# Kernel optimization log

Hardware: AMD Instinct MI355X
Metric: run time of the kernel (lower is better)

Reference implementation:

```python
import jax, jax.numpy as jnp
import numpy as np

D_MODEL = 1024


def setup_inputs() -> dict:
    key = jax.random.key(0)
    ks = jax.random.split(key, 7)
    s = 1.0 / np.sqrt(D_MODEL)
    return {
        "x": jax.random.normal(ks[0], (4, 4096, D_MODEL), dtype=jnp.float32),
        "Wq": jax.random.normal(ks[1], (D_MODEL, D_MODEL), dtype=jnp.float32) * s,
        "bq": jax.random.normal(ks[2], (D_MODEL,), dtype=jnp.float32) * s,
        "Wk": jax.random.normal(ks[3], (D_MODEL, D_MODEL), dtype=jnp.float32) * s,
        "bk": jax.random.normal(ks[4], (D_MODEL,), dtype=jnp.float32) * s,
        "Wv": jax.random.normal(ks[5], (D_MODEL, D_MODEL), dtype=jnp.float32) * s,
        "bv": jax.random.normal(ks[6], (D_MODEL,), dtype=jnp.float32) * s,
    }


def reference(x, Wq, bq, Wk, bk, Wv, bv):
    # nn.Linear: y = x @ W.T + b
    Q = jnp.einsum("bsd,ed->bse", x, Wq) + bq  # [B,S,D]
    K = jnp.einsum("bsd,ed->bse", x, Wk) + bk
    V = jnp.einsum("bsd,ed->bse", x, Wv) + bv
    scale = 1.0 / jnp.sqrt(jnp.asarray(x.shape[-1], dtype=x.dtype))
    KV = jnp.einsum("bsd,bse->bde", K, V) * scale  # [B,D,D]
    E = jnp.einsum("bsd,bde->bse", Q, KV)  # [B,S,D]
    return E
```

## Files before the change

### kernel.cpp

```cpp
#include <hip/hip_runtime.h>
#include <hip/hip_fp16.h>


#define BATCH 4
#define SEQ   4096
#define DM    1024

typedef _Float16 h8 __attribute__((ext_vector_type(8)));
typedef _Float16 h4 __attribute__((ext_vector_type(4)));
typedef float    f4 __attribute__((ext_vector_type(4)));

__device__ inline void gload_lds16(const _Float16* g, _Float16* l) {
    __builtin_amdgcn_global_load_lds(
        (const __attribute__((address_space(1))) void*)g,
        (__attribute__((address_space(3))) void*)l,
        16, 0, 0);
}

__device__ inline int xcd_swz(int bid, int grid) {
    const int q = grid >> 3;
    return (bid & 7) * q + (bid >> 3);
}

__device__ inline float doth(const _Float16* wr, const float* v, int lane) {
    float s = 0.f;
    #pragma unroll
    for (int i = 0; i < 2; ++i) {
        const int k = i * 512 + lane * 8;
        h8 wv = *(const h8*)&wr[k];
        f4 v0 = *(const f4*)&v[k];
        f4 v1 = *(const f4*)&v[k + 4];
        s += (float)wv[0] * v0.x + (float)wv[1] * v0.y +
             (float)wv[2] * v0.z + (float)wv[3] * v0.w +
             (float)wv[4] * v1.x + (float)wv[5] * v1.y +
             (float)wv[6] * v1.z + (float)wv[7] * v1.w;
    }
    return s;
}
__device__ inline void doth4(const _Float16* wr, const float* xs, int lane, float* s) {
    #pragma unroll
    for (int i = 0; i < 2; ++i) {
        const int k = i * 512 + lane * 8;
        h8 wv = *(const h8*)&wr[k];
        #pragma unroll
        for (int b = 0; b < 4; ++b) {
            const float* v = xs + b * DM + k;
            f4 v0 = *(const f4*)&v[0];
            f4 v1 = *(const f4*)&v[4];
            s[b] += (float)wv[0] * v0.x + (float)wv[1] * v0.y +
                    (float)wv[2] * v0.z + (float)wv[3] * v0.w +
                    (float)wv[4] * v1.x + (float)wv[5] * v1.y +
                    (float)wv[6] * v1.z + (float)wv[7] * v1.w;
        }
    }
}
__device__ inline float dotf(const float* a, const float* b, int lane) {
    float s = 0.f;
    #pragma unroll
    for (int i = 0; i < 4; ++i) {
        const int k = i * 256 + lane * 4;
        f4 x = *(const f4*)&a[k];
        f4 y = *(const f4*)&b[k];
        s += x.x * y.x + x.y * y.y + x.z * y.z + x.w * y.w;
    }
    return s;
}
__device__ inline float wred(float s) {
    #pragma unroll
    for (int off = 32; off; off >>= 1) s += __shfl_down(s, off);
    return s;
}

__global__ __launch_bounds__(256) void cvt_all(
    const float* __restrict__ x, const float* __restrict__ Wq,
    const float* __restrict__ Wk, const float* __restrict__ Wv,
    _Float16* __restrict__ xt, _Float16* __restrict__ xh,
    _Float16* __restrict__ Wqt, _Float16* __restrict__ Wkt,
    _Float16* __restrict__ Wvh, float* __restrict__ xs)
{
    __shared__ float tile[64][65];
    __shared__ float red[4][64];
    const int bid = blockIdx.x;
    const int t   = threadIdx.x;
    const int tr  = t >> 4;
    const int tc  = (t & 15) * 4;

    const float* src;
    _Float16 *dstT = nullptr, *dstRM = nullptr;
    int r0, c0, C, R;
    bool isX = bid < 4096;
    if (isX) {
        const int b  = bid >> 10;
        const int tt = bid & 1023;
        r0 = (tt >> 4) * 64; c0 = (tt & 15) * 64;
        R = SEQ; C = DM;
        src   = x  + (long)b * SEQ * DM;
        dstT  = xt + (long)b * SEQ * DM;
        dstRM = xh + (long)b * SEQ * DM;
        xs   += b * DM;
    } else {
        const int wb = bid - 4096;
        const int z  = wb >> 8;
        const int tt = wb & 255;
        r0 = (tt >> 4) * 64; c0 = (tt & 15) * 64;
        R = DM; C = DM;
        src = z == 0 ? Wq : (z == 1 ? Wk : Wv);
        if (z == 0) dstT = Wqt;
        else if (z == 1) dstT = Wkt;
        else dstRM = Wvh;
    }

    #pragma unroll
    for (int i = 0; i < 4; ++i) {
        const int r = tr + i * 16;
        f4 v = *(const f4*)&src[(long)(r0 + r) * C + c0 + tc];
        tile[r][tc + 0] = v.x; tile[r][tc + 1] = v.y;
        tile[r][tc + 2] = v.z; tile[r][tc + 3] = v.w;
        if (dstRM) {
            h4 h = { (_Float16)v.x, (_Float16)v.y, (_Float16)v.z, (_Float16)v.w };
            *(h4*)&dstRM[(long)(r0 + r) * C + c0 + tc] = h;
        }
    }
    __syncthreads();
    if (dstT) {
        #pragma unroll
        for (int i = 0; i < 4; ++i) {
            const int c = tr + i * 16;
            h4 h = { (_Float16)tile[tc + 0][c], (_Float16)tile[tc + 1][c],
                     (_Float16)tile[tc + 2][c], (_Float16)tile[tc + 3][c] };
            *(h4*)&dstT[(long)(c0 + c) * R + r0 + tc] = h;
        }
    }
    if (isX) {
        const int cc = t & 63;
        const int rb = (t >> 6) * 16;
        float ps = 0.f;
        #pragma unroll
        for (int r = 0; r < 16; ++r) ps += tile[rb + r][cc];
        red[t >> 6][cc] = ps;
        __syncthreads();
        if (t < 64)
            atomicAdd(&xs[c0 + t], red[0][t] + red[1][t] + red[2][t] + red[3][t]);
    }
}

__global__ __launch_bounds__(256) void gemv_misc(
    const _Float16* __restrict__ Wvh, const _Float16* __restrict__ Wqt,
    const _Float16* __restrict__ Wkt,
    const float* __restrict__ xs, const float* __restrict__ bv,
    const float* __restrict__ bk, const float* __restrict__ bq,
    float* __restrict__ u2, float* __restrict__ qk,
    float* __restrict__ kb)
{
    const int gw   = blockIdx.x * 4 + (threadIdx.x >> 6);
    const int lane = threadIdx.x & 63;
    if (gw < 1024) {
        float s[4] = {};
        doth4(Wvh + (long)gw * DM, xs, lane, s);
        #pragma unroll
        for (int b = 0; b < 4; ++b) {
            float r = wred(s[b]);
            if (lane == 0) u2[b * DM + gw] = r + (float)SEQ * bv[gw];
        }
    } else if (gw < 2048) {
        float s = wred(doth(Wqt + (long)(gw - 1024) * DM, bk, lane));
        if (lane == 0) qk[gw - 1024] = s;
    } else if (gw < 3072) {
        float s = wred(doth(Wkt + (long)(gw - 2048) * DM, bq, lane));
        if (lane == 0) kb[gw - 2048] = s;
    }
}

__global__ __launch_bounds__(256) void gemv_cvqw(
    const _Float16* __restrict__ Ph, const _Float16* __restrict__ Mh,
    const float* __restrict__ kb, const float* __restrict__ xs,
    const float* __restrict__ u2, const float* __restrict__ bv,
    const float* __restrict__ sv,
    float* __restrict__ cv, float* __restrict__ qw)
{
    const int gw   = blockIdx.x * 4 + (threadIdx.x >> 6);
    const int lane = threadIdx.x & 63;
    if (gw < 4096) {
        const int b = gw >> 10;
        const int e = gw & 1023;
        float s = wred(doth(Ph + (long)b * DM * DM + (long)e * DM, kb, lane));
        if (lane == 0)
            cv[gw] = s + (sv[0] * u2[gw] + sv[1 + b] * bv[e]) * 0.03125f;
    } else if (gw < 5120) {
        const int i = gw - 4096;
        float s[4] = {};
        doth4(Mh + (long)i * DM, xs, lane, s);
        #pragma unroll
        for (int b = 0; b < 4; ++b) {
            float r = wred(s[b]);
            if (lane == 0) qw[b * DM + i] = r;
        }
    }
}

__global__ __launch_bounds__(256) void reduce_tri(
    const _Float16* __restrict__ parts, _Float16* __restrict__ Gh,
    const float* __restrict__ kb, const float* __restrict__ xs,
    const float* __restrict__ bq, const float* __restrict__ bk,
    float* __restrict__ sv)
{
    const int bid = blockIdx.x;
    if (bid == 640) {
        const int wv   = threadIdx.x >> 6;
        const int lane = threadIdx.x & 63;
        float s = wred(dotf(kb, xs + wv * DM, lane));
        if (lane == 0) sv[1 + wv] = s;
        if (wv == 0) {
            float s0 = wred(dotf(bq, bk, lane));
            if (lane == 0) sv[0] = s0;
        }
        return;
    }
    __shared__ _Float16 lds[64][72];
    const int job = bid >> 4;
    const int ch  = bid & 15;
    const int b   = job / 10;
    const int p   = job - b * 10;
    const int ti  = p >= 6 ? 3 : (p >= 3 ? 2 : (p >= 1 ? 1 : 0));
    const int tj  = p - ((ti * (ti + 1)) >> 1);
    const int li  = (ch >> 2) * 64;
    const int lj  = (ch & 3) * 64;
    const int t   = threadIdx.x;
    const int c8  = (t & 7) * 8;
    const long DD_ = (long)DM * DM;

    h8 o[2];
    #pragma unroll
    for (int h = 0; h < 2; ++h) {
        const int r = (t >> 3) + h * 32;
        float a[8] = {};
        #pragma unroll
        for (int s = 0; s < 6; ++s) {
            const _Float16* src = parts + ((long)(job * 6 + s) << 16);
            h8 v = *(const h8*)&src[(li + r) * 256 + lj + c8];
            #pragma unroll
            for (int j = 0; j < 8; ++j) a[j] += (float)v[j];
        }
        #pragma unroll
        for (int j = 0; j < 8; ++j) o[h][j] = (_Float16)(a[j] * 0.03125f);
        *(h8*)&Gh[b * DD_ + (long)(ti * 256 + li + r) * DM + tj * 256 + lj + c8] = o[h];
        *(h8*)&lds[r][c8] = o[h];
    }
    if (ti != tj) {
        __syncthreads();
        #pragma unroll
        for (int h = 0; h < 2; ++h) {
            const int r = (t >> 3) + h * 32;
            h8 m;
            #pragma unroll
            for (int j = 0; j < 8; ++j) m[j] = lds[c8 + j][r];
            *(h8*)&Gh[b * DD_ + (long)(tj * 256 + lj + r) * DM + ti * 256 + li + c8] = m;
        }
    }
}

template<typename OutT, int BIAS, int TRI>
__global__ __launch_bounds__(512, 1) void gemm8p(
    const _Float16* __restrict__ A, const _Float16* __restrict__ B,
    OutT* __restrict__ C,
    int K, int lda, int ldb, int ldc, int tilesX, int perZ,
    long aZ, long bZ, long cZ, int sk, long aK, long bK,
    const float* __restrict__ bc1, long bc1Z, float alpha)
{
    __shared__ _Float16 lds[2 * 32768];

    const int L = xcd_swz(blockIdx.x, gridDim.x);
    int tileM, tileN, cTileM, cTileN, NT;
    const float* pc1 = nullptr;
    if (TRI) {
        const int job = L / 6;
        const int s   = L - job * 6;
        const int b   = job / 10;
        const int p   = job - b * 10;
        const int ti  = p >= 6 ? 3 : (p >= 3 ? 2 : (p >= 1 ? 1 : 0));
        const int tj  = p - ((ti * (ti + 1)) >> 1);
        const int kOff = s < 4 ? s * 704 : 2816 + (s - 4) * 640;
        NT = s < 4 ? 11 : 10;
        A += (long)b * aZ + kOff;
        B += (long)b * aZ + kOff;
        C += (long)(job * 6 + s) * cZ;
        tileM = ti * 256; tileN = tj * 256;
        cTileM = 0; cTileN = 0;
    } else {
        const int z  = L / perZ;
        const int r0 = L - z * perZ;
        const int zb = z / sk;
        const int zk = z - zb * sk;
        A += (long)zb * aZ + (long)zk * aK;
        B += (long)zb * bZ + (long)zk * bK;
        C += (long)z * cZ;
        if (BIAS == 1) pc1 = bc1 + (long)zb * bc1Z;
        tileM = (r0 / tilesX) * 256;
        tileN = (r0 % tilesX) * 256;
        cTileM = tileM; cTileN = tileN;
        NT = K >> 6;
    }

    const int tid  = threadIdx.x;
    const int lane = tid & 63;
    const int wave = tid >> 6;
    const int wr   = wave >> 2;
    const int wc   = wave & 3;
    const int la   = lane & 15;
    const int kg   = lane >> 4;

    auto stageA = [&](int buf, int mq, int kt) {
        _Float16* dst = &lds[buf * 32768 + mq * 8192];
        const int k0 = kt * 64;
        #pragma unroll
        for (int i = 0; i < 2; ++i) {
            const int U = i * 512 + tid;
            const int R = U >> 3, s = U & 7;
            const int gr = tileM + (R >> 6) * 128 + mq * 64 + (R & 63);
            gload_lds16(&A[(long)gr * lda + k0 + ((s ^ (R & 7)) << 3)], dst + U * 8);
        }
    };
    auto stageB = [&](int buf, int nq, int kt) {
        _Float16* dst = &lds[buf * 32768 + 16384 + nq * 8192];
        const int k0 = kt * 64;
        #pragma unroll
        for (int i = 0; i < 2; ++i) {
            const int U = i * 512 + tid;
            const int R = U >> 3, s = U & 7;
            const int gn = tileN + (R >> 5) * 64 + nq * 32 + (R & 31);
            gload_lds16(&B[(long)gn * ldb + k0 + ((s ^ (R & 7)) << 3)], dst + U * 8);
        }
    };

    f4 acc[8][4] = {};
    h8 af[4][2];
    h8 bf[2][2][2];

    auto readA = [&](int buf, int mq) {
        const _Float16* Ab = &lds[buf * 32768 + mq * 8192];
        #pragma unroll
        for (int mi = 0; mi < 4; ++mi)
            #pragma unroll
            for (int kk = 0; kk < 2; ++kk) {
                const int R = wr * 64 + mi * 16 + la;
                const int s = kk * 4 + kg;
                af[mi][kk] = *(const h8*)&Ab[R * 64 + ((s ^ (R & 7)) << 3)];
            }
    };
    auto readB = [&](int buf, int nq) {
        const _Float16* Bb = &lds[buf * 32768 + 16384 + nq * 8192];
        #pragma unroll
        for (int ni = 0; ni < 2; ++ni)
            #pragma unroll
            for (int kk = 0; kk < 2; ++kk) {
                const int R = wc * 32 + ni * 16 + la;
                const int s = kk * 4 + kg;
                bf[nq][ni][kk] = *(const h8*)&Bb[R * 64 + ((s ^ (R & 7)) << 3)];
            }
    };
    auto mfmaQ = [&](int mq, int nq) {
        __builtin_amdgcn_s_setprio(1);
        #pragma unroll
        for (int mi = 0; mi < 4; ++mi)
            #pragma unroll
            for (int ni = 0; ni < 2; ++ni)
                #pragma unroll
                for (int kk = 0; kk < 2; ++kk)
                    acc[mq * 4 + mi][nq * 2 + ni] =
                        __builtin_amdgcn_mfma_f32_16x16x32_f16(
                            af[mi][kk], bf[nq][ni][kk],
                            acc[mq * 4 + mi][nq * 2 + ni], 0, 0, 0);
        __builtin_amdgcn_s_setprio(0);
    };

    stageA(0, 0, 0); stageA(0, 1, 0); stageB(0, 0, 0); stageB(0, 1, 0);
    if (NT > 1) {
        stageA(1, 0, 1); stageB(1, 0, 1);
        asm volatile("s_waitcnt vmcnt(4)" ::: "memory");
    } else {
        asm volatile("s_waitcnt vmcnt(0)" ::: "memory");
    }
    __builtin_amdgcn_sched_barrier(0);
    __builtin_amdgcn_s_barrier();
    readB(0, 0);

    for (int j = 0; j < NT; ++j) {
        const int buf = j & 1;
        readA(buf, 0);
        if (j + 1 < NT) stageA(buf ^ 1, 1, j + 1);
        __builtin_amdgcn_s_barrier();
        asm volatile("s_waitcnt lgkmcnt(0)" ::: "memory");
        __builtin_amdgcn_sched_barrier(0);
        mfmaQ(0, 0);
        __builtin_amdgcn_s_barrier();
        readB(buf, 1);
        if (j + 1 < NT) stageB(buf ^ 1, 1, j + 1);
        __builtin_amdgcn_s_barrier();
        asm volatile("s_waitcnt lgkmcnt(0)" ::: "memory");
        __builtin_amdgcn_sched_barrier(0);
        mfmaQ(0, 1);
        __builtin_amdgcn_s_barrier();
        readA(buf, 1);
        if (j + 2 < NT) stageA(buf, 0, j + 2);
        __builtin_amdgcn_s_barrier();
        asm volatile("s_waitcnt lgkmcnt(0)" ::: "memory");
        __builtin_amdgcn_sched_barrier(0);
        mfmaQ(1, 0);
        if (j + 2 < NT) {
            asm volatile("s_waitcnt vmcnt(6)" ::: "memory");
        } else if (j + 1 < NT) {
            asm volatile("s_waitcnt vmcnt(4)" ::: "memory");
        }
        __builtin_amdgcn_sched_barrier(0);
        __builtin_amdgcn_s_barrier();
        if (j + 1 < NT) readB(buf ^ 1, 0);
        if (j + 2 < NT) stageB(buf, 0, j + 2);
        __builtin_amdgcn_s_barrier();
        mfmaQ(1, 1);
        if (j + 2 < NT) {
            asm volatile("s_waitcnt vmcnt(4)" ::: "memory");
        } else if (j + 1 < NT) {
            asm volatile("s_waitcnt vmcnt(0)" ::: "memory");
        }
        __builtin_amdgcn_sched_barrier(0);
        __builtin_amdgcn_s_barrier();
    }

    #pragma unroll
    for (int mf = 0; mf < 8; ++mf) {
        #pragma unroll
        for (int nf = 0; nf < 4; ++nf) {
            const int col = cTileN + wc * 64 + nf * 16 + la;
            #pragma unroll
            for (int jj = 0; jj < 4; ++jj) {
                const int row = cTileM + wr * 128 + mf * 16 + kg * 4 + jj;
                float v = acc[mf][nf][jj] * alpha;
                if (BIAS == 1) v += pc1[col];
                C[(long)row * ldc + col] = (OutT)v;
            }
        }
    }
}

template<int BIAS>
__global__ __launch_bounds__(256) void gemm64(
    const _Float16* __restrict__ A, const _Float16* __restrict__ B,
    _Float16* __restrict__ C,
    const _Float16* __restrict__ A2, const _Float16* __restrict__ B2,
    _Float16* __restrict__ C2, int zSplit,
    int K, int lda, int ldb, int ldc, int tilesX, int perZ,
    long aZ, long bZ, long cZ,
    const float* __restrict__ bc1, long bc1Z,
    const float* __restrict__ br1, long br1Z,
    const float* __restrict__ bc2, long bc2Z,
    const float* __restrict__ br2, long br2Z,
    float alpha, float beta)
{
    __shared__ _Float16 As[64 * 64];
    __shared__ _Float16 Bs[64 * 64];

    const int L  = xcd_swz(blockIdx.x, gridDim.x);
    int z        = L / perZ;
    const int r0 = L - z * perZ;
    if (z >= zSplit) { A = A2; B = B2; C = C2; z = 0; }
    A += (long)z * aZ;
    B += (long)z * bZ;
    C += (long)z * cZ;
    const float* pc1 = nullptr; const float* pr1 = nullptr;
    const float* pc2 = nullptr; const float* pr2 = nullptr;
    if (BIAS == 3) {
        pc1 = bc1 + (long)z * bc1Z; pr1 = br1 + (long)z * br1Z;
        pc2 = bc2 + (long)z * bc2Z; pr2 = br2 + (long)z * br2Z;
    }

    const int tileM = (r0 / tilesX) * 64;
    const int tileN = (r0 % tilesX) * 64;
    const int tid   = threadIdx.x;
    const int lane  = tid & 63;
    const int wave  = tid >> 6;
    const int wm    = (wave >> 1) * 32;
    const int wn    = (wave & 1) * 32;
    const int srow  = tid >> 3;
    const int sslot = tid & 7;

    f4 acc[2][2] = {};
    const int arow = lane & 15;
    const int kg   = lane >> 4;

    for (int k0 = 0; k0 < K; k0 += 64) {
        #pragma unroll
        for (int i = 0; i < 2; ++i) {
            const int row   = i * 32 + srow;
            const int gslot = sslot ^ (row & 7);
            gload_lds16(&A[(long)(tileM + row) * lda + k0 + gslot * 8],
                        &As[row * 64 + sslot * 8]);
            gload_lds16(&B[(long)(tileN + row) * ldb + k0 + gslot * 8],
                        &Bs[row * 64 + sslot * 8]);
        }
        __syncthreads();

        #pragma unroll
        for (int kk = 0; kk < 64; kk += 32) {
            h8 af[2], bf[2];
            #pragma unroll
            for (int m = 0; m < 2; ++m) {
                const int rr   = wm + m * 16 + arow;
                const int slot = (kk >> 3) + kg;
                af[m] = *(const h8*)&As[rr * 64 + ((slot ^ (rr & 7)) << 3)];
            }
            #pragma unroll
            for (int n = 0; n < 2; ++n) {
                const int rr   = wn + n * 16 + arow;
                const int slot = (kk >> 3) + kg;
                bf[n] = *(const h8*)&Bs[rr * 64 + ((slot ^ (rr & 7)) << 3)];
            }
            #pragma unroll
            for (int m = 0; m < 2; ++m)
                #pragma unroll
                for (int n = 0; n < 2; ++n)
                    acc[m][n] = __builtin_amdgcn_mfma_f32_16x16x32_f16(
                        af[m], bf[n], acc[m][n], 0, 0, 0);
        }
        __syncthreads();
    }

    #pragma unroll
    for (int m = 0; m < 2; ++m) {
        #pragma unroll
        for (int n = 0; n < 2; ++n) {
            const int col = tileN + wn + n * 16 + arow;
            #pragma unroll
            for (int j = 0; j < 4; ++j) {
                const int row = tileM + wm + m * 16 + (lane >> 4) * 4 + j;
                float v = acc[m][n][j] * alpha;
                if (BIAS == 3) v += beta * (pc1[col] * pr1[row] + pc2[col] * pr2[row]);
                C[(long)row * ldc + col] = (_Float16)v;
            }
        }
    }
}

extern "C" void kernel_launch(void* const* d_in, const int* in_sizes, int n_in,
                              void* d_out, int out_size, void* d_ws, size_t ws_size,
                              hipStream_t stream)
{
    const float* x  = (const float*)d_in[0];
    const float* Wq = (const float*)d_in[1];
    const float* bq = (const float*)d_in[2];
    const float* Wk = (const float*)d_in[3];
    const float* bk = (const float*)d_in[4];
    const float* Wv = (const float*)d_in[5];
    const float* bv = (const float*)d_in[6];
    float* out = (float*)d_out;

    const long DD = (long)DM * DM;
    const long DS = (long)DM * SEQ;
    const long MB = 1024l * 1024;

    char* base = (char*)d_ws;
    _Float16* xh   = (_Float16*)base;
    _Float16* xt   = (_Float16*)(base + 32 * MB);
    _Float16* Gh   = xt;
    _Float16* Ph   = (_Float16*)(base + 40 * MB);
    _Float16* Rth  = (_Float16*)(base + 48 * MB);
    _Float16* Wqt  = (_Float16*)(base + 64 * MB);
    _Float16* Wvh  = (_Float16*)(base + 66 * MB);
    _Float16* Wkt  = (_Float16*)(base + 68 * MB);
    _Float16* Mh   = (_Float16*)(base + 70 * MB);
    float*    vecs = (float*)(base + 72 * MB);
    float*    u2   = vecs;
    float*    qk   = vecs + 4096;
    float*    kb   = vecs + 5120;
    float*    xs   = vecs + 6144;
    float*    qw   = vecs + 10240;
    float*    cv   = vecs + 14336;
    float*    sv   = vecs + 18432;
    _Float16* parts = (_Float16*)d_out;

    hipMemsetAsync(xs, 0, BATCH * DM * sizeof(float), stream);

    cvt_all<<<4864, 256, 0, stream>>>(x, Wq, Wk, Wv, xt, xh, Wqt, Wkt, Wvh, xs);

    gemv_misc<<<768, 256, 0, stream>>>(Wvh, Wqt, Wkt, xs, bv, bk, bq, u2, qk, kb);

    gemm8p<_Float16, 0, 1><<<240, 512, 0, stream>>>(
        xt, xt, parts, 4096, SEQ, SEQ, 256, 0, 0,
        DS, DS, 65536, 1, 0, 0, nullptr, 0, 1.0f);

    reduce_tri<<<641, 256, 0, stream>>>(parts, Gh, kb, xs, bq, bk, sv);

    gemm64<0><<<1280, 256, 0, stream>>>(
        Wvh, Gh, Ph, Wqt, Wkt, Mh, 4,
        1024, DM, DM, DM, 16, 256,
        0, DD, DD,
        nullptr, 0, nullptr, 0, nullptr, 0, nullptr, 0, 1.0f, 0.f);

    gemv_cvqw<<<1280, 256, 0, stream>>>(Ph, Mh, kb, xs, u2, bv, sv, cv, qw);

    gemm64<3><<<1024, 256, 0, stream>>>(
        Ph, Mh, Rth, nullptr, nullptr, nullptr, 99,
        1024, DM, DM, DM, 16, 256,
        DD, 0, DD,
        qk, 0, u2, 1024, qw, 1024, bv, 0, 1.0f, 0.03125f);

    gemm8p<float, 1, 0><<<256, 512, 0, stream>>>(
        xh, Rth, out, 1024, DM, DM, DM, 4, 64,
        DS, DD, DS, 1, 0, 0, cv, 1024, 1.0f);
}
```

Baseline: 152.0 us.

## Eliminate gemv_cvqw launch by refactoring qw via Wk and fusing cv into gemm64

qw is now computed as Wq^T·(Wk·xs). The inner product runs in gemv_misc using a new row-major fp16 copy of Wk, and the outer one runs in extra blocks of reduce_tri, so it no longer depends on Mh. The cv GEMV is folded into extra blocks of the gemm64<3> launch, which removes a separate kernel launch and dependency. The gemm8p main loop also moves the B-fragment LDS reads to the top of each iteration and drops one vmcnt wait/barrier pair, which changes the software pipelining. In exchange the code writes an extra 2MB fp16 weight copy and runs two chained GEMVs, and the reordered waits risk hazards.

After: 151.3 us. About the same (-0.4%).

```diff
diff --git a/kernel.cpp b/kernel.cpp
--- a/kernel.cpp
+++ b/kernel.cpp
@@ -76,7 +76,8 @@
     const float* __restrict__ Wk, const float* __restrict__ Wv,
     _Float16* __restrict__ xt, _Float16* __restrict__ xh,
     _Float16* __restrict__ Wqt, _Float16* __restrict__ Wkt,
-    _Float16* __restrict__ Wvh, float* __restrict__ xs)
+    _Float16* __restrict__ Wkh, _Float16* __restrict__ Wvh,
+    float* __restrict__ xs)
 {
     __shared__ float tile[64][65];
     __shared__ float red[4][64];
@@ -105,8 +106,8 @@
         r0 = (tt >> 4) * 64; c0 = (tt & 15) * 64;
         R = DM; C = DM;
         src = z == 0 ? Wq : (z == 1 ? Wk : Wv);
-        if (z == 0) dstT = Wqt;
-        else if (z == 1) dstT = Wkt;
+        if (z == 0) { dstT = Wqt; }
+        else if (z == 1) { dstT = Wkt; dstRM = Wkh; }
         else dstRM = Wvh;
     }
 
@@ -146,11 +147,11 @@
 
 __global__ __launch_bounds__(256) void gemv_misc(
     const _Float16* __restrict__ Wvh, const _Float16* __restrict__ Wqt,
-    const _Float16* __restrict__ Wkt,
+    const _Float16* __restrict__ Wkt, const _Float16* __restrict__ Wkh,
     const float* __restrict__ xs, const float* __restrict__ bv,
     const float* __restrict__ bk, const float* __restrict__ bq,
     float* __restrict__ u2, float* __restrict__ qk,
-    float* __restrict__ kb)
+    float* __restrict__ kb, float* __restrict__ w)
 {
     const int gw   = blockIdx.x * 4 + (threadIdx.x >> 6);
     const int lane = threadIdx.x & 63;
@@ -168,51 +169,45 @@
     } else if (gw < 3072) {
         float s = wred(doth(Wkt + (long)(gw - 2048) * DM, bq, lane));
         if (lane == 0) kb[gw - 2048] = s;
-    }
-}
-
-__global__ __launch_bounds__(256) void gemv_cvqw(
-    const _Float16* __restrict__ Ph, const _Float16* __restrict__ Mh,
-    const float* __restrict__ kb, const float* __restrict__ xs,
-    const float* __restrict__ u2, const float* __restrict__ bv,
-    const float* __restrict__ sv,
-    float* __restrict__ cv, float* __restrict__ qw)
-{
-    const int gw   = blockIdx.x * 4 + (threadIdx.x >> 6);
-    const int lane = threadIdx.x & 63;
-    if (gw < 4096) {
-        const int b = gw >> 10;
-        const int e = gw & 1023;
-        float s = wred(doth(Ph + (long)b * DM * DM + (long)e * DM, kb, lane));
-        if (lane == 0)
-            cv[gw] = s + (sv[0] * u2[gw] + sv[1 + b] * bv[e]) * 0.03125f;
-    } else if (gw < 5120) {
-        const int i = gw - 4096;
+    } else {
+        const int d = gw - 3072;
         float s[4] = {};
-        doth4(Mh + (long)i * DM, xs, lane, s);
+        doth4(Wkh + (long)d * DM, xs, lane, s);
         #pragma unroll
         for (int b = 0; b < 4; ++b) {
             float r = wred(s[b]);
-            if (lane == 0) qw[b * DM + i] = r;
+            if (lane == 0) w[b * DM + d] = r;
         }
     }
 }
 
 __global__ __launch_bounds__(256) void reduce_tri(
     const _Float16* __restrict__ parts, _Float16* __restrict__ Gh,
+    const _Float16* __restrict__ Wqt, const float* __restrict__ w,
     const float* __restrict__ kb, const float* __restrict__ xs,
     const float* __restrict__ bq, const float* __restrict__ bk,
-    float* __restrict__ sv)
+    float* __restrict__ qw, float* __restrict__ sv)
 {
     const int bid = blockIdx.x;
-    if (bid == 640) {
+    if (bid >= 640) {
         const int wv   = threadIdx.x >> 6;
         const int lane = threadIdx.x & 63;
-        float s = wred(dotf(kb, xs + wv * DM, lane));
-        if (lane == 0) sv[1 + wv] = s;
-        if (wv == 0) {
-            float s0 = wred(dotf(bq, bk, lane));
-            if (lane == 0) sv[0] = s0;
+        if (bid < 896) {
+            const int i = (bid - 640) * 4 + wv;
+            float s[4] = {};
+            doth4(Wqt + (long)i * DM, w, lane, s);
+            #pragma unroll
+            for (int b = 0; b < 4; ++b) {
+                float r = wred(s[b]);
+                if (lane == 0) qw[b * DM + i] = r;
+            }
+        } else {
+            float s = wred(dotf(kb, xs + wv * DM, lane));
+            if (lane == 0) sv[1 + wv] = s;
+            if (wv == 0) {
+                float s0 = wred(dotf(bq, bk, lane));
+                if (lane == 0) sv[0] = s0;
+            }
         }
         return;
     }
@@ -382,12 +377,12 @@
     }
     __builtin_amdgcn_sched_barrier(0);
     __builtin_amdgcn_s_barrier();
-    readB(0, 0);
 
     for (int j = 0; j < NT; ++j) {
         const int buf = j & 1;
-        readA(buf, 0);
+        readA(buf, 0); readB(buf, 0);
         if (j + 1 < NT) stageA(buf ^ 1, 1, j + 1);
+        asm volatile("s_waitcnt lgkmcnt(8)" ::: "memory");
         __builtin_amdgcn_s_barrier();
         asm volatile("s_waitcnt lgkmcnt(0)" ::: "memory");
         __builtin_amdgcn_sched_barrier(0);
@@ -406,14 +401,7 @@
         asm volatile("s_waitcnt lgkmcnt(0)" ::: "memory");
         __builtin_amdgcn_sched_barrier(0);
         mfmaQ(1, 0);
-        if (j + 2 < NT) {
-            asm volatile("s_waitcnt vmcnt(6)" ::: "memory");
-        } else if (j + 1 < NT) {
-            asm volatile("s_waitcnt vmcnt(4)" ::: "memory");
-        }
-        __builtin_amdgcn_sched_barrier(0);
-        __builtin_amdgcn_s_barrier();
-        if (j + 1 < NT) readB(buf ^ 1, 0);
+        __builtin_amdgcn_s_barrier();
         if (j + 2 < NT) stageB(buf, 0, j + 2);
         __builtin_amdgcn_s_barrier();
         mfmaQ(1, 1);
@@ -462,7 +450,40 @@
     const int L  = xcd_swz(blockIdx.x, gridDim.x);
     int z        = L / perZ;
     const int r0 = L - z * perZ;
-    if (z >= zSplit) { A = A2; B = B2; C = C2; z = 0; }
+    if (z >= zSplit) {
+        if (BIAS == 3) {
+            const float* kb = (const float*)A2;
+            const float* sv = (const float*)B2;
+            float*       cv = (float*)C2;
+            const int wv   = threadIdx.x >> 6;
+            const int lane = threadIdx.x & 63;
+            const int e    = (L - zSplit * perZ) * 4 + wv;
+            float s[4] = {};
+            #pragma unroll
+            for (int i = 0; i < 2; ++i) {
+                const int k = i * 512 + lane * 8;
+                f4 k0 = *(const f4*)&kb[k];
+                f4 k1 = *(const f4*)&kb[k + 4];
+                #pragma unroll
+                for (int b = 0; b < 4; ++b) {
+                    h8 pv = *(const h8*)&A[(long)b * aZ + (long)e * lda + k];
+                    s[b] += (float)pv[0] * k0.x + (float)pv[1] * k0.y +
+                            (float)pv[2] * k0.z + (float)pv[3] * k0.w +
+                            (float)pv[4] * k1.x + (float)pv[5] * k1.y +
+                            (float)pv[6] * k1.z + (float)pv[7] * k1.w;
+                }
+            }
+            #pragma unroll
+            for (int b = 0; b < 4; ++b) {
+                float r = wred(s[b]);
+                if (lane == 0)
+                    cv[b * DM + e] = r + (sv[0] * br1[b * br1Z + e] +
+                                          sv[1 + b] * br2[e]) * 0.03125f;
+            }
+            return;
+        }
+        A = A2; B = B2; C = C2; z = 0;
+    }
     A += (long)z * aZ;
     B += (long)z * bZ;
     C += (long)z * cZ;
@@ -566,8 +587,9 @@
     _Float16* Wqt  = (_Float16*)(base + 64 * MB);
     _Float16* Wvh  = (_Float16*)(base + 66 * MB);
     _Float16* Wkt  = (_Float16*)(base + 68 * MB);
-    _Float16* Mh   = (_Float16*)(base + 70 * MB);
-    float*    vecs = (float*)(base + 72 * MB);
+    _Float16* Wkh  = (_Float16*)(base + 70 * MB);
+    _Float16* Mh   = (_Float16*)(base + 72 * MB);
+    float*    vecs = (float*)(base + 74 * MB);
     float*    u2   = vecs;
     float*    qk   = vecs + 4096;
     float*    kb   = vecs + 5120;
@@ -575,19 +597,21 @@
     float*    qw   = vecs + 10240;
     float*    cv   = vecs + 14336;
     float*    sv   = vecs + 18432;
+    float*    w    = vecs + 20480;
     _Float16* parts = (_Float16*)d_out;
 
     hipMemsetAsync(xs, 0, BATCH * DM * sizeof(float), stream);
 
-    cvt_all<<<4864, 256, 0, stream>>>(x, Wq, Wk, Wv, xt, xh, Wqt, Wkt, Wvh, xs);
-
-    gemv_misc<<<768, 256, 0, stream>>>(Wvh, Wqt, Wkt, xs, bv, bk, bq, u2, qk, kb);
+    cvt_all<<<4864, 256, 0, stream>>>(x, Wq, Wk, Wv, xt, xh, Wqt, Wkt, Wkh, Wvh, xs);
+
+    gemv_misc<<<1024, 256, 0, stream>>>(Wvh, Wqt, Wkt, Wkh, xs, bv, bk, bq,
+                                        u2, qk, kb, w);
 
     gemm8p<_Float16, 0, 1><<<240, 512, 0, stream>>>(
         xt, xt, parts, 4096, SEQ, SEQ, 256, 0, 0,
         DS, DS, 65536, 1, 0, 0, nullptr, 0, 1.0f);
 
-    reduce_tri<<<641, 256, 0, stream>>>(parts, Gh, kb, xs, bq, bk, sv);
+    reduce_tri<<<897, 256, 0, stream>>>(parts, Gh, Wqt, w, kb, xs, bq, bk, qw, sv);
 
     gemm64<0><<<1280, 256, 0, stream>>>(
         Wvh, Gh, Ph, Wqt, Wkt, Mh, 4,
@@ -595,10 +619,9 @@
         0, DD, DD,
         nullptr, 0, nullptr, 0, nullptr, 0, nullptr, 0, 1.0f, 0.f);
 
-    gemv_cvqw<<<1280, 256, 0, stream>>>(Ph, Mh, kb, xs, u2, bv, sv, cv, qw);
-
-    gemm64<3><<<1024, 256, 0, stream>>>(
-        Ph, Mh, Rth, nullptr, nullptr, nullptr, 99,
+    gemm64<3><<<1280, 256, 0, stream>>>(
+        Ph, Mh, Rth,
+        (const _Float16*)kb, (const _Float16*)sv, (_Float16*)cv, 4,
         1024, DM, DM, DM, 16, 256,
         DD, 0, DD,
         qk, 0, u2, 1024, qw, 1024, bv, 0, 1.0f, 0.03125f);
```
